# Kernel tuning notes

Hardware: AMD Instinct MI355X
Metric: run time of the kernel (lower is better)

Reference implementation:

```python
import jax, jax.numpy as jnp
import numpy as np

B, L, D = 2, 2048, 2048
H, HD = 16, 128
E = 8192
SCALE = float(np.sqrt(HD))


def setup_inputs() -> dict:
    key = jax.random.key(0)
    ks = jax.random.split(key, 8)
    s = 0.02
    x = jax.random.normal(ks[0], (B, L, D), dtype=jnp.float32)
    # causal mask: True where key position j > query position i (masked out)
    mask = jnp.triu(jnp.ones((L, L), dtype=bool), k=1)
    Wq = jax.random.normal(ks[1], (D, D), dtype=jnp.float32) * s
    Wk = jax.random.normal(ks[2], (D, D), dtype=jnp.float32) * s
    Wv = jax.random.normal(ks[3], (D, D), dtype=jnp.float32) * s
    W1 = jax.random.normal(ks[4], (D, E), dtype=jnp.float32) * s
    Vg = jax.random.normal(ks[5], (D, E), dtype=jnp.float32) * s
    W2 = jax.random.normal(ks[6], (E, D), dtype=jnp.float32) * s
    return {"x": x, "mask": mask, "Wq": Wq, "Wk": Wk, "Wv": Wv,
            "W1": W1, "Vg": Vg, "W2": W2}


def reynolds_fn(s):
    # Reynolds (group-averaging) operator over key axis: blend score with its row mean
    return 0.5 * s + 0.5 * jnp.mean(s, axis=-1, keepdims=True)


def reference(x, mask, Wq, Wk, Wv, W1, Vg, W2):
    b, l, d = x.shape
    q = (x @ Wq).reshape(b, l, H, HD).transpose(0, 2, 1, 3)  # (B,H,L,hd)
    k = (x @ Wk).reshape(b, l, H, HD).transpose(0, 2, 1, 3)
    v = (x @ Wv).reshape(b, l, H, HD).transpose(0, 2, 1, 3)
    scores = jnp.einsum('bhqd,bhkd->bhqk', q, k) / SCALE
    scores = reynolds_fn(scores)
    scores = jnp.where(mask[None, None], -jnp.inf, scores)
    attn = jax.nn.softmax(scores, axis=-1)
    out = jnp.einsum('bhqk,bhkd->bhqd', attn, v)
    out = out.transpose(0, 2, 1, 3).reshape(b, l, d)  # (B,L,D)
    h = jax.nn.silu(out @ W1) * (out @ Vg)  # SwiGLU
    return h @ W2
```

## Files before the change

kernel.cpp:

```cpp
#include <hip/hip_runtime.h>
#include <stdint.h>

typedef unsigned short u16;
typedef __attribute__((ext_vector_type(8))) short bf16x8;
typedef __attribute__((ext_vector_type(4))) float f32x4;

#define DEVINL static __device__ __forceinline__

DEVINL void gload_lds16(const void* g, void* l) {
  __builtin_amdgcn_global_load_lds(
      (const __attribute__((address_space(1))) unsigned int*)g,
      (__attribute__((address_space(3))) unsigned int*)l, 16, 0, 0);
}

DEVINL u16 f2b(float f) {
  union { float f; unsigned u; } v; v.f = f;
  unsigned r = (v.u + 0x7FFFu + ((v.u >> 16) & 1u)) >> 16;
  return (u16)r;
}

DEVINL bf16x8 ldsv8(const u16* p) { return *(const bf16x8*)p; }

DEVINL void topw6() { asm volatile("s_waitcnt vmcnt(6)\n\ts_barrier" ::: "memory"); }
DEVINL void topw8() { asm volatile("s_waitcnt vmcnt(8)\n\ts_barrier" ::: "memory"); }
DEVINL void topw0() { asm volatile("s_waitcnt vmcnt(0)\n\ts_barrier" ::: "memory"); }
DEVINL void midw()  { asm volatile("s_waitcnt lgkmcnt(0)\n\ts_barrier" ::: "memory"); }

__global__ __launch_bounds__(256) void convt_f32_bf16(
    const float* __restrict__ in, u16* __restrict__ out, int R, int C) {
  __shared__ u16 t[64][65];
  const int c0 = blockIdx.x * 64, r0 = blockIdx.y * 64;
  const int tx = threadIdx.x & 63, ty = threadIdx.x >> 6;
#pragma unroll
  for (int i = 0; i < 64; i += 4)
    t[ty + i][tx] = f2b(in[(size_t)(r0 + ty + i) * C + c0 + tx]);
  __syncthreads();
#pragma unroll
  for (int i = 0; i < 64; i += 4)
    out[(size_t)(c0 + ty + i) * R + r0 + tx] = t[tx][ty + i];
}

__global__ __launch_bounds__(256) void conv_f32_bf16(
    const float* __restrict__ in, u16* __restrict__ out) {
  const size_t i = ((size_t)blockIdx.x * 256 + threadIdx.x) * 4;
  const float4 v = *(const float4*)(in + i);
  ushort4 o;
  o.x = f2b(v.x); o.y = f2b(v.y); o.z = f2b(v.z); o.w = f2b(v.w);
  *(ushort4*)(out + i) = o;
}

template <int EPI>
__global__ __launch_bounds__(512, 2) void gemm_bt(
    const u16* __restrict__ A, const u16* __restrict__ B1,
    const u16* __restrict__ B2, u16* __restrict__ C, float* __restrict__ Cf,
    u16* __restrict__ Ck, u16* __restrict__ Cv,
    int M, int N, int K) {
  constexpr bool DUAL = (EPI == 2);
  constexpr int NG = DUAL ? 8 : 6;
  constexpr int OFF_B = 16384;
  constexpr int OFF_B2 = 24576;
  constexpr int BUFU = DUAL ? 32768 : 24576;
  extern __shared__ __align__(16) u16 sL[];

  const int tid = threadIdx.x;
  const int w = tid >> 6, lane = tid & 63;
  const int ln = lane & 15, quad = lane >> 4;
  const int wm = (w >> 1) << 6;
  const int wn = (w & 1) << 6;
  const size_t m0 = (size_t)blockIdx.y * 256;
  const size_t n0 = (size_t)blockIdx.x * 128;

  const int srow = lane >> 3;
  const int scol = (((lane & 7) ^ srow) << 3);
  const int xc0 = ((quad ^ (ln & 7)) << 3);
  const int xc1 = (((4 + quad) ^ (ln & 7)) << 3);

  const u16* gp[NG];
  int ldo[NG];
#pragma unroll
  for (int i = 0; i < 4; ++i) {
    const int j = (w << 2) + i;
    gp[i] = A + (m0 + (size_t)(j * 8 + srow)) * K + scol;
    ldo[i] = j << 9;
  }
#pragma unroll
  for (int i = 0; i < 2; ++i) {
    const int j = (w << 1) + i;
    gp[4 + i] = B1 + (n0 + (size_t)(j * 8 + srow)) * K + scol;
    ldo[4 + i] = OFF_B + (j << 9);
  }
  if constexpr (DUAL) {
#pragma unroll
    for (int i = 0; i < 2; ++i) {
      const int j = (w << 1) + i;
      gp[6 + i] = B2 + (n0 + (size_t)(j * 8 + srow)) * K + scol;
      ldo[6 + i] = OFF_B2 + (j << 9);
    }
  }

  const f32x4 z4 = {0.f, 0.f, 0.f, 0.f};
  f32x4 acc[4][4];
  f32x4 acc2[DUAL ? 4 : 1][DUAL ? 4 : 1];
#pragma unroll
  for (int i = 0; i < 4; ++i)
#pragma unroll
    for (int j = 0; j < 4; ++j) {
      acc[i][j] = z4;
      if constexpr (DUAL) acc2[i][j] = z4;
    }

  auto stageT = [&](int tt, int buf) {
    const size_t ko = (size_t)tt << 6;
#pragma unroll
    for (int j = 0; j < NG; ++j)
      gload_lds16(gp[j] + ko, &sL[buf * BUFU + ldo[j]]);
  };

  auto ldf = [&](const u16* base, int xc, bf16x8* a, bf16x8* b, bf16x8* c2) {
#pragma unroll
    for (int mi = 0; mi < 4; ++mi)
      a[mi] = ldsv8(base + (wm + mi * 16 + ln) * 64 + xc);
#pragma unroll
    for (int ni = 0; ni < 4; ++ni)
      b[ni] = ldsv8(base + OFF_B + (wn + ni * 16 + ln) * 64 + xc);
    if constexpr (DUAL) {
#pragma unroll
      for (int ni = 0; ni < 4; ++ni)
        c2[ni] = ldsv8(base + OFF_B2 + (wn + ni * 16 + ln) * 64 + xc);
    }
  };

  auto mf = [&](const bf16x8* a, const bf16x8* b, const bf16x8* c2) {
    __builtin_amdgcn_s_setprio(1);
#pragma unroll
    for (int ni = 0; ni < 4; ++ni) {
#pragma unroll
      for (int mi = 0; mi < 4; ++mi) {
        acc[mi][ni] =
            __builtin_amdgcn_mfma_f32_16x16x32_bf16(a[mi], b[ni], acc[mi][ni], 0, 0, 0);
        if constexpr (DUAL)
          acc2[mi][ni] =
              __builtin_amdgcn_mfma_f32_16x16x32_bf16(a[mi], c2[ni], acc2[mi][ni], 0, 0, 0);
      }
    }
    __builtin_amdgcn_s_setprio(0);
  };

  auto body = [&](int t, bool do_stage) {
    const u16* base = &sL[(t & 1) * BUFU];
    bf16x8 a[4], b[4], c2[DUAL ? 4 : 1];
    ldf(base, xc0, a, b, c2);
    mf(a, b, c2);
    ldf(base, xc1, a, b, c2);
    midw();
    if (do_stage) stageT(t + 2, t & 1);
    mf(a, b, c2);
  };

  const int nkt = K >> 6;
  stageT(0, 0);
  stageT(1, 1);
  for (int t = 0; t < nkt - 1; ++t) {
    if constexpr (DUAL) topw8(); else topw6();
    body(t, t < nkt - 2);
  }
  topw0();
  body(nkt - 1, false);

#pragma unroll
  for (int mi = 0; mi < 4; ++mi)
#pragma unroll
    for (int ni = 0; ni < 4; ++ni)
#pragma unroll
      for (int r = 0; r < 4; ++r) {
        const size_t rg = m0 + wm + mi * 16 + quad * 4 + r;
        const size_t cg = n0 + wn + ni * 16 + ln;
        const float v = acc[mi][ni][r];
        if constexpr (EPI == 0) {
          Cf[rg * N + cg] = v;
        } else if constexpr (EPI == 4) {
          const size_t b = rg >> 11, l = rg & 2047;
          const size_t c = cg & 2047, h = c >> 7, hd = c & 127;
          const int which = (int)(cg >> 11);
          if (which == 0)
            C[(((b << 4) + h) * 2048 + l) * 128 + hd] = f2b(v);
          else if (which == 1)
            Ck[(((b << 4) + h) * 2048 + l) * 128 + hd] = f2b(v);
          else
            Cv[(((b << 4) + h) * 128 + hd) * 2048 + l] = f2b(v);
        } else {
          const float v2 = acc2[mi][ni][r];
          const float s = v / (1.f + __expf(-v));
          C[rg * N + cg] = f2b(s * v2);
        }
      }
}

__global__ __launch_bounds__(256, 2) void attn(
    const u16* __restrict__ Q, const u16* __restrict__ Km,
    const u16* __restrict__ VT, u16* __restrict__ O) {
  constexpr int L = 2048, HD = 128, QT = 128, KT = 64;
  __shared__ __align__(16) u16 sQ[QT * HD];
  __shared__ __align__(16) u16 sKP[QT * KT];
  __shared__ __align__(16) u16 sV[HD * KT];

  const int bh = blockIdx.y;
  const int q0 = blockIdx.x * QT;
  const int tid = threadIdx.x, w = tid >> 6, lane = tid & 63;
  const int ln = lane & 15, quad = lane >> 4;
  const int wr = w * 32;

  const u16* Qb = Q + (size_t)bh * L * HD + (size_t)q0 * HD;
  const u16* Kb = Km + (size_t)bh * L * HD;
  const u16* Vb = VT + (size_t)bh * HD * L;

#pragma unroll
  for (int i = 0; i < 8; ++i) {
    const int j = w * 8 + i;
    const int row = j * 4 + (lane >> 4);
    const int c = (lane & 15) ^ (row & 15);
    gload_lds16(Qb + row * HD + c * 8, &sQ[j * 512]);
  }

  const f32x4 z4 = {0.f, 0.f, 0.f, 0.f};
  float l_st[2][4];
  f32x4 accO[2][8];
#pragma unroll
  for (int mi = 0; mi < 2; ++mi) {
#pragma unroll
    for (int r = 0; r < 4; ++r) l_st[mi][r] = 0.f;
#pragma unroll
    for (int nt = 0; nt < 8; ++nt) accO[mi][nt] = z4;
  }

  const float scale = 0.04419417382415922f;
  const int nkt = (q0 >> 6) + 2;

  for (int kt = 0; kt < nkt; ++kt) {
    const int kb = kt << 6;
    __syncthreads();
#pragma unroll
    for (int i = 0; i < 4; ++i) {
      const int j = (w << 2) + i;
      const int krow = j * 4 + (lane >> 4);
      const int kc = (lane & 15) ^ (krow & 15);
      gload_lds16(Kb + (size_t)(kb + krow) * HD + kc * 8, &sKP[j * 512]);
      const int vrow = (j << 3) + (lane >> 3);
      const int vc = (lane & 7) ^ (lane >> 3);
      gload_lds16(Vb + (size_t)vrow * L + kb + vc * 8, &sV[j * 512]);
    }
    __syncthreads();

    f32x4 accS[2][4];
#pragma unroll
    for (int mi = 0; mi < 2; ++mi)
#pragma unroll
      for (int ct = 0; ct < 4; ++ct) accS[mi][ct] = z4;
#pragma unroll
    for (int kk = 0; kk < 4; ++kk) {
      const int xc = (((kk << 2) + quad) ^ ln) << 3;
      bf16x8 aq[2];
#pragma unroll
      for (int mi = 0; mi < 2; ++mi)
        aq[mi] = ldsv8(&sQ[(wr + mi * 16 + ln) * HD + xc]);
#pragma unroll
      for (int ct = 0; ct < 4; ++ct) {
        bf16x8 bk = ldsv8(&sKP[(ct * 16 + ln) * HD + xc]);
#pragma unroll
        for (int mi = 0; mi < 2; ++mi)
          accS[mi][ct] =
              __builtin_amdgcn_mfma_f32_16x16x32_bf16(aq[mi], bk, accS[mi][ct], 0, 0, 0);
      }
    }
    __syncthreads();

    const bool maskt = (kb + KT > q0);
#pragma unroll
    for (int mi = 0; mi < 2; ++mi) {
#pragma unroll
      for (int r = 0; r < 4; ++r) {
        const int qrow = q0 + wr + mi * 16 + quad * 4 + r;
        const int prow = wr + mi * 16 + quad * 4 + r;
        float sum = 0.f;
#pragma unroll
        for (int ct = 0; ct < 4; ++ct) {
          float e = __expf(accS[mi][ct][r] * scale);
          if (maskt && (kb + ct * 16 + ln > qrow)) e = 0.f;
          sum += e;
          const int pc = (ct * 2 + (ln >> 3)) ^ (prow & 7);
          sKP[prow * KT + pc * 8 + (ln & 7)] = f2b(e);
        }
        sum += __shfl_xor(sum, 1);
        sum += __shfl_xor(sum, 2);
        sum += __shfl_xor(sum, 4);
        sum += __shfl_xor(sum, 8);
        l_st[mi][r] += sum;
      }
    }
    __syncthreads();

#pragma unroll
    for (int kk = 0; kk < 2; ++kk) {
      const int xc = (((kk << 2) + quad) ^ (ln & 7)) << 3;
      bf16x8 ap[2];
#pragma unroll
      for (int mi = 0; mi < 2; ++mi)
        ap[mi] = ldsv8(&sKP[(wr + mi * 16 + ln) * KT + xc]);
#pragma unroll
      for (int nt = 0; nt < 8; ++nt) {
        bf16x8 bv = ldsv8(&sV[(nt * 16 + ln) * KT + xc]);
#pragma unroll
        for (int mi = 0; mi < 2; ++mi)
          accO[mi][nt] =
              __builtin_amdgcn_mfma_f32_16x16x32_bf16(ap[mi], bv, accO[mi][nt], 0, 0, 0);
      }
    }
  }

  const int b = bh >> 4, h = bh & 15;
#pragma unroll
  for (int mi = 0; mi < 2; ++mi)
#pragma unroll
    for (int nt = 0; nt < 8; ++nt)
#pragma unroll
      for (int r = 0; r < 4; ++r) {
        const int qrow = q0 + wr + mi * 16 + quad * 4 + r;
        const float v = accO[mi][nt][r] / l_st[mi][r];
        O[(size_t)(b * 2048 + qrow) * 2048 + h * 128 + nt * 16 + ln] = f2b(v);
      }
}

extern "C" void kernel_launch(void* const* d_in, const int* in_sizes, int n_in,
                              void* d_out, int out_size, void* d_ws, size_t ws_size,
                              hipStream_t stream) {
  const float* x  = (const float*)d_in[0];
  const float* Wq = (const float*)d_in[2];
  const float* Wk = (const float*)d_in[3];
  const float* Wv = (const float*)d_in[4];
  const float* W1 = (const float*)d_in[5];
  const float* Vg = (const float*)d_in[6];
  const float* W2 = (const float*)d_in[7];
  float* out = (float*)d_out;
  char* ws = (char*)d_ws;

  const size_t MB = 1ull << 20;
  u16* W1T = (u16*)(ws);
  u16* VgT = (u16*)(ws + 32 * MB);
  u16* W2T = (u16*)(ws + 64 * MB);
  u16* WqT = (u16*)(ws + 96 * MB);
  u16* WkT = (u16*)(ws + 104 * MB);
  u16* WvT = (u16*)(ws + 112 * MB);
  u16* xb  = (u16*)(ws + 120 * MB);
  u16* Qb  = (u16*)(ws + 136 * MB);
  u16* Kb  = (u16*)(ws + 152 * MB);
  u16* VTb = (u16*)(ws + 168 * MB);
  u16* Ob  = (u16*)(ws + 184 * MB);
  u16* Hb  = (u16*)(ws + 96 * MB);

  constexpr int LDS_S = 2 * 24576 * 2;
  constexpr int LDS_D = 2 * 32768 * 2;
  (void)hipFuncSetAttribute((const void*)gemm_bt<4>,
                            hipFuncAttributeMaxDynamicSharedMemorySize, LDS_S);
  (void)hipFuncSetAttribute((const void*)gemm_bt<2>,
                            hipFuncAttributeMaxDynamicSharedMemorySize, LDS_D);
  (void)hipFuncSetAttribute((const void*)gemm_bt<0>,
                            hipFuncAttributeMaxDynamicSharedMemorySize, LDS_S);

  dim3 blk(256), gblk(512);
  convt_f32_bf16<<<dim3(32, 32), blk, 0, stream>>>(Wq, WqT, 2048, 2048);
  convt_f32_bf16<<<dim3(32, 32), blk, 0, stream>>>(Wk, WkT, 2048, 2048);
  convt_f32_bf16<<<dim3(32, 32), blk, 0, stream>>>(Wv, WvT, 2048, 2048);
  convt_f32_bf16<<<dim3(128, 32), blk, 0, stream>>>(W1, W1T, 2048, 8192);
  convt_f32_bf16<<<dim3(128, 32), blk, 0, stream>>>(Vg, VgT, 2048, 8192);
  convt_f32_bf16<<<dim3(32, 128), blk, 0, stream>>>(W2, W2T, 8192, 2048);
  conv_f32_bf16<<<dim3(8192), blk, 0, stream>>>(x, xb);

  gemm_bt<4><<<dim3(48, 16), gblk, LDS_S, stream>>>(
      xb, WqT, nullptr, Qb, nullptr, Kb, VTb, 4096, 6144, 2048);

  attn<<<dim3(16, 32), blk, 0, stream>>>(Qb, Kb, VTb, Ob);

  gemm_bt<2><<<dim3(64, 16), gblk, LDS_D, stream>>>(
      Ob, W1T, VgT, Hb, nullptr, nullptr, nullptr, 4096, 8192, 2048);

  gemm_bt<0><<<dim3(16, 16), gblk, LDS_S, stream>>>(
      Hb, W2T, nullptr, nullptr, out, nullptr, nullptr, 4096, 2048, 8192);
}
```

Measured before the change: 874.0 us.

## Switch GEMM to triple-buffered LDS pipeline with one barrier per K-tile

Replaces the two-slot LDS scheme with three slots for the A tile (and for B in the single-B GEMM). The next-next tile is now issued right after the top-of-loop barrier, so the mid-iteration lgkmcnt wait and barrier go away. In the dual-B GEMM, A is triple-buffered and the two B tiles are double-buffered and staged one step ahead, which keeps LDS within the budget. The aim is fewer barriers and more load/compute overlap, at the cost of larger dynamic LDS (up to 160 KB for the dual variant) and tighter vmcnt bookkeeping.

```diff
diff --git a/kernel.cpp b/kernel.cpp
--- a/kernel.cpp
+++ b/kernel.cpp
@@ -21,10 +21,9 @@
 
 DEVINL bf16x8 ldsv8(const u16* p) { return *(const bf16x8*)p; }
 
-DEVINL void topw6() { asm volatile("s_waitcnt vmcnt(6)\n\ts_barrier" ::: "memory"); }
-DEVINL void topw8() { asm volatile("s_waitcnt vmcnt(8)\n\ts_barrier" ::: "memory"); }
-DEVINL void topw0() { asm volatile("s_waitcnt vmcnt(0)\n\ts_barrier" ::: "memory"); }
-DEVINL void midw()  { asm volatile("s_waitcnt lgkmcnt(0)\n\ts_barrier" ::: "memory"); }
+DEVINL void vmb6() { asm volatile("s_waitcnt vmcnt(6)\n\ts_barrier" ::: "memory"); }
+DEVINL void vmb4() { asm volatile("s_waitcnt vmcnt(4)\n\ts_barrier" ::: "memory"); }
+DEVINL void vmb0() { asm volatile("s_waitcnt vmcnt(0)\n\ts_barrier" ::: "memory"); }
 
 __global__ __launch_bounds__(256) void convt_f32_bf16(
     const float* __restrict__ in, u16* __restrict__ out, int R, int C) {
@@ -56,10 +55,6 @@
     u16* __restrict__ Ck, u16* __restrict__ Cv,
     int M, int N, int K) {
   constexpr bool DUAL = (EPI == 2);
-  constexpr int NG = DUAL ? 8 : 6;
-  constexpr int OFF_B = 16384;
-  constexpr int OFF_B2 = 24576;
-  constexpr int BUFU = DUAL ? 32768 : 24576;
   extern __shared__ __align__(16) u16 sL[];
 
   const int tid = threadIdx.x;
@@ -75,26 +70,28 @@
   const int xc0 = ((quad ^ (ln & 7)) << 3);
   const int xc1 = (((4 + quad) ^ (ln & 7)) << 3);
 
-  const u16* gp[NG];
-  int ldo[NG];
+  const u16* gpA[4];
+  int loA[4];
 #pragma unroll
   for (int i = 0; i < 4; ++i) {
     const int j = (w << 2) + i;
-    gp[i] = A + (m0 + (size_t)(j * 8 + srow)) * K + scol;
-    ldo[i] = j << 9;
-  }
+    gpA[i] = A + (m0 + (size_t)(j * 8 + srow)) * K + scol;
+    loA[i] = j << 9;
+  }
+  const u16* gpB[2];
+  int loB[2];
 #pragma unroll
   for (int i = 0; i < 2; ++i) {
     const int j = (w << 1) + i;
-    gp[4 + i] = B1 + (n0 + (size_t)(j * 8 + srow)) * K + scol;
-    ldo[4 + i] = OFF_B + (j << 9);
-  }
+    gpB[i] = B1 + (n0 + (size_t)(j * 8 + srow)) * K + scol;
+    loB[i] = j << 9;
+  }
+  const u16* gpB2[DUAL ? 2 : 1];
   if constexpr (DUAL) {
 #pragma unroll
     for (int i = 0; i < 2; ++i) {
       const int j = (w << 1) + i;
-      gp[6 + i] = B2 + (n0 + (size_t)(j * 8 + srow)) * K + scol;
-      ldo[6 + i] = OFF_B2 + (j << 9);
+      gpB2[i] = B2 + (n0 + (size_t)(j * 8 + srow)) * K + scol;
     }
   }
 
@@ -109,31 +106,43 @@
       if constexpr (DUAL) acc2[i][j] = z4;
     }
 
-  auto stageT = [&](int tt, int buf) {
+  auto stageA = [&](int tt, int slot) {
     const size_t ko = (size_t)tt << 6;
-#pragma unroll
-    for (int j = 0; j < NG; ++j)
-      gload_lds16(gp[j] + ko, &sL[buf * BUFU + ldo[j]]);
+    const int base = DUAL ? slot * 16384 : slot * 24576;
+#pragma unroll
+    for (int j = 0; j < 4; ++j) gload_lds16(gpA[j] + ko, &sL[base + loA[j]]);
   };
-
-  auto ldf = [&](const u16* base, int xc, bf16x8* a, bf16x8* b, bf16x8* c2) {
+  auto stageB = [&](int tt, int slot) {
+    const size_t ko = (size_t)tt << 6;
+    if constexpr (!DUAL) {
+      const int base = slot * 24576 + 16384;
+#pragma unroll
+      for (int j = 0; j < 2; ++j) gload_lds16(gpB[j] + ko, &sL[base + loB[j]]);
+    } else {
+      const int b1 = 49152 + slot * 8192, b2 = 65536 + slot * 8192;
+#pragma unroll
+      for (int j = 0; j < 2; ++j) gload_lds16(gpB[j] + ko, &sL[b1 + loB[j]]);
+#pragma unroll
+      for (int j = 0; j < 2; ++j) gload_lds16(gpB2[j] + ko, &sL[b2 + loB[j]]);
+    }
+  };
+
+  auto halfK = [&](const u16* Ab, const u16* Bb, const u16* B2b, int xc) {
+    bf16x8 a[4], b[4], c2[DUAL ? 4 : 1];
 #pragma unroll
     for (int mi = 0; mi < 4; ++mi)
-      a[mi] = ldsv8(base + (wm + mi * 16 + ln) * 64 + xc);
+      a[mi] = ldsv8(Ab + (wm + mi * 16 + ln) * 64 + xc);
 #pragma unroll
     for (int ni = 0; ni < 4; ++ni)
-      b[ni] = ldsv8(base + OFF_B + (wn + ni * 16 + ln) * 64 + xc);
+      b[ni] = ldsv8(Bb + (wn + ni * 16 + ln) * 64 + xc);
     if constexpr (DUAL) {
 #pragma unroll
       for (int ni = 0; ni < 4; ++ni)
-        c2[ni] = ldsv8(base + OFF_B2 + (wn + ni * 16 + ln) * 64 + xc);
-    }
-  };
-
-  auto mf = [&](const bf16x8* a, const bf16x8* b, const bf16x8* c2) {
+        c2[ni] = ldsv8(B2b + (wn + ni * 16 + ln) * 64 + xc);
+    }
     __builtin_amdgcn_s_setprio(1);
 #pragma unroll
-    for (int ni = 0; ni < 4; ++ni) {
+    for (int ni = 0; ni < 4; ++ni)
 #pragma unroll
       for (int mi = 0; mi < 4; ++mi) {
         acc[mi][ni] =
@@ -142,30 +151,40 @@
           acc2[mi][ni] =
               __builtin_amdgcn_mfma_f32_16x16x32_bf16(a[mi], c2[ni], acc2[mi][ni], 0, 0, 0);
       }
-    }
     __builtin_amdgcn_s_setprio(0);
   };
 
-  auto body = [&](int t, bool do_stage) {
-    const u16* base = &sL[(t & 1) * BUFU];
-    bf16x8 a[4], b[4], c2[DUAL ? 4 : 1];
-    ldf(base, xc0, a, b, c2);
-    mf(a, b, c2);
-    ldf(base, xc1, a, b, c2);
-    midw();
-    if (do_stage) stageT(t + 2, t & 1);
-    mf(a, b, c2);
-  };
-
   const int nkt = K >> 6;
-  stageT(0, 0);
-  stageT(1, 1);
-  for (int t = 0; t < nkt - 1; ++t) {
-    if constexpr (DUAL) topw8(); else topw6();
-    body(t, t < nkt - 2);
-  }
-  topw0();
-  body(nkt - 1, false);
+  if constexpr (!DUAL) {
+    stageA(0, 0); stageB(0, 0);
+    stageA(1, 1); stageB(1, 1);
+  } else {
+    stageA(0, 0); stageB(0, 0);
+    stageA(1, 1);
+  }
+
+  int s3 = 0, sn = 2;
+  for (int t = 0; t < nkt; ++t) {
+    if (t == nkt - 1) vmb0();
+    else if constexpr (DUAL) vmb4();
+    else vmb6();
+
+    if constexpr (!DUAL) {
+      if (t + 2 < nkt) { stageA(t + 2, sn); stageB(t + 2, sn); }
+    } else {
+      if (t + 1 < nkt) stageB(t + 1, (t + 1) & 1);
+      if (t + 2 < nkt) stageA(t + 2, sn);
+    }
+
+    const u16* Ab = &sL[DUAL ? s3 * 16384 : s3 * 24576];
+    const u16* Bb = DUAL ? &sL[49152 + (t & 1) * 8192] : Ab + 16384;
+    const u16* B2b = DUAL ? &sL[65536 + (t & 1) * 8192] : Ab;
+    halfK(Ab, Bb, B2b, xc0);
+    halfK(Ab, Bb, B2b, xc1);
+
+    s3 = (s3 == 2) ? 0 : s3 + 1;
+    sn = (sn == 2) ? 0 : sn + 1;
+  }
 
 #pragma unroll
   for (int mi = 0; mi < 4; ++mi)
@@ -357,8 +376,8 @@
   u16* Ob  = (u16*)(ws + 184 * MB);
   u16* Hb  = (u16*)(ws + 96 * MB);
 
-  constexpr int LDS_S = 2 * 24576 * 2;
-  constexpr int LDS_D = 2 * 32768 * 2;
+  constexpr int LDS_S = 3 * 24576 * 2;
+  constexpr int LDS_D = 81920 * 2;
   (void)hipFuncSetAttribute((const void*)gemm_bt<4>,
                             hipFuncAttributeMaxDynamicSharedMemorySize, LDS_S);
   (void)hipFuncSetAttribute((const void*)gemm_bt<2>,
```

Result: slower. 906.1 us (+3.7%).
